# Performance work log

Measured on AMD Instinct MI355X. Metric: run time of the kernel, lower is better.

Reference implementation:

```python
import jax, jax.numpy as jnp
import numpy as np

H = 64      # hidden width of each MLP
M_STEPS = 64   # SDE steps (m)
N_SIM = 2048   # Monte-Carlo paths (n)
D = 128        # number of options (data_size)


def _mlp4(x, W1, b1, W2, b2, W3, b3):
    # x: [n, d, 4]; weights stacked over the 4 networks on axis 0 (k)
    h = jax.nn.relu(jnp.einsum('ndf,kfh->kndh', x, W1) + b1[:, None, None, :])
    h = jax.nn.relu(jnp.einsum('kndh,khg->kndg', h, W2) + b2[:, None, None, :])
    o = jnp.einsum('kndg,kgo->kndo', h, W3) + b3[:, None, None, :]
    return jnp.tanh(o)  # [4, n, d, 1]


def setup_inputs() -> dict:
    key = jax.random.key(0)
    ks = jax.random.split(key, 12)
    S0 = jax.random.uniform(ks[0], (D,), jnp.float32, 50.0, 150.0)
    K = jax.random.uniform(ks[1], (D,), jnp.float32, 50.0, 150.0)
    T = jax.random.uniform(ks[2], (D,), jnp.float32, 0.25, 2.0)
    rf = jnp.array([0.03], jnp.float32)
    V0 = jnp.array([0.04], jnp.float32)
    rho = jnp.array([-0.5], jnp.float32)
    Z1 = jax.random.normal(ks[3], (M_STEPS, N_SIM, D), jnp.float32)
    Z2raw = jax.random.normal(ks[4], (M_STEPS, N_SIM, D), jnp.float32)
    # 4 MLPs, layers [4, H, H, 1]
    W1 = jax.random.normal(ks[5], (4, 4, H), jnp.float32) / jnp.sqrt(4.0)
    b1 = jnp.zeros((4, H), jnp.float32)
    W2 = jax.random.normal(ks[6], (4, H, H), jnp.float32) / jnp.sqrt(float(H))
    b2 = jnp.zeros((4, H), jnp.float32)
    W3 = jax.random.normal(ks[7], (4, H, 1), jnp.float32) / jnp.sqrt(float(H))
    b3 = jnp.zeros((4, 1), jnp.float32)
    return {"S0": S0, "K": K, "T": T, "rf": rf, "V0": V0, "rho": rho,
            "Z1": Z1, "Z2raw": Z2raw,
            "W1": W1, "b1": b1, "W2": W2, "b2": b2, "W3": W3, "b3": b3}


def reference(S0, K, T, rf, V0, rho, Z1, Z2raw, W1, b1, W2, b2, W3, b3):
    m, n, d = Z1.shape
    dt = (T / m)[None, :, None]          # [1, d, 1]
    sdt = jnp.sqrt(dt)
    rho_s = rho[0]
    rf_s = rf[0]
    S = jnp.broadcast_to(S0[None, :, None], (n, d, 1))
    V = jnp.broadcast_to(V0[0], (n, d, 1))

    def step(carry, xs):
        S, V = carry
        j, z1, z2r = xs                    # z1, z2r: [n, d]
        z2 = rho_s * z1 + jnp.sqrt(1.0 - rho_s ** 2) * z2r
        feat = jnp.concatenate([
            S, V,
            jnp.broadcast_to(rf_s, S.shape),
            jnp.broadcast_to(dt * j, S.shape),
        ], axis=2)                          # [n, d, 4]
        N1, N2, N3, N4 = _mlp4(feat, W1, b1, W2, b2, W3, b3)
        Vn = V * (1.0 + N3 * dt + N4 * sdt * z2[..., None])
        Sn = S * (1.0 + N1 * dt + N2 * sdt * z1[..., None])
        return (Sn, Vn), None

    js = jnp.arange(m, dtype=jnp.float32)
    (S, V), _ = jax.lax.scan(step, (S, V), (js, Z1, Z2raw))
    S = S[..., 0]                            # [n, d]
    payoff = jnp.maximum(S - K[None, :], 0.0)
    P_pred = jnp.sum(jnp.exp(-rf_s * T)[None, :] * payoff, axis=0) / n
    return P_pred
```

## Files before the change

### kernel.cpp

```cpp
#include <hip/hip_runtime.h>
#include <math.h>

#define D_OPT   128
#define N_SIM   2048
#define M_STEPS 64
#define HID     64


typedef _Float16 f16x8 __attribute__((ext_vector_type(8)));
typedef _Float16 f16x2 __attribute__((ext_vector_type(2)));
typedef float    f32x4 __attribute__((ext_vector_type(4)));
typedef unsigned int u32;
typedef u32 u32x4 __attribute__((ext_vector_type(4)));

__device__ __forceinline__ u32 pk2u(float a, float b) {
#if __has_builtin(__builtin_amdgcn_cvt_pkrtz)
    return __builtin_bit_cast(u32, __builtin_amdgcn_cvt_pkrtz(a, b));
#else
    f16x2 p; p[0] = (_Float16)a; p[1] = (_Float16)b;
    return __builtin_bit_cast(u32, p);
#endif
}

__device__ __forceinline__ u32 pk_relu_cvt(float a, float b) {
    f16x2 p = __builtin_bit_cast(f16x2, pk2u(a, b));
    const f16x2 z = { (_Float16)0.0f, (_Float16)0.0f };
#if __has_builtin(__builtin_elementwise_max)
    p = __builtin_elementwise_max(p, z);
#else
    p[0] = p[0] > z[0] ? p[0] : z[0];
    p[1] = p[1] > z[1] ? p[1] : z[1];
#endif
    return __builtin_bit_cast(u32, p);
}

__global__ __launch_bounds__(256, 2) void nsde_kernel(
    const float* __restrict__ S0p, const float* __restrict__ Kp,
    const float* __restrict__ Tp,  const float* __restrict__ rfp,
    const float* __restrict__ V0p, const float* __restrict__ rhop,
    const float* __restrict__ Z1,  const float* __restrict__ Z2r,
    const float* __restrict__ W1,  const float* __restrict__ B1,
    const float* __restrict__ W2,  const float* __restrict__ B2,
    const float* __restrict__ W3,  const float* __restrict__ B3,
    float* __restrict__ out)
{
    __shared__ f32x4 nv_lds[2][64];
    __shared__ uint2 pkx[4][64];

    const int tid  = threadIdx.x;
    const int wave = tid >> 6;
    const int lane = tid & 63;
    const int q    = lane >> 4;
    const int mA   = lane & 15;
    const float rf = rfp[0];

    const float* w1g = W1 + wave * 256;
    const float* b1g = B1 + wave * 64;
    const float* w2g = W2 + wave * 4096;
    const float* b2g = B2 + wave * 64;
    const float* w3g = W3 + wave * 64;

    f16x8 A1[4];
    #pragma unroll
    for (int t = 0; t < 4; ++t) {
        f16x8 a;
        #pragma unroll
        for (int j = 0; j < 8; ++j) a[j] = (_Float16)0.0f;
        if (q == 0) {
            const int h = t * 16 + mA;
            a[0] = (_Float16)w1g[0 * 64 + h];
            a[1] = (_Float16)w1g[1 * 64 + h];
            a[2] = (_Float16)w1g[3 * 64 + h];
        }
        A1[t] = a;
    }

    f16x8 A2[4][2];
    #pragma unroll
    for (int gt = 0; gt < 4; ++gt)
        #pragma unroll
        for (int kt = 0; kt < 2; ++kt) {
            f16x8 a;
            #pragma unroll
            for (int j = 0; j < 8; ++j) {
                const int h1 = (2 * kt + (j >> 2)) * 16 + 4 * q + (j & 3);
                a[j] = (_Float16)w2g[h1 * 64 + gt * 16 + mA];
            }
            A2[gt][kt] = a;
        }

    f16x8 A3[2];
    #pragma unroll
    for (int kt = 0; kt < 2; ++kt) {
        f16x8 a;
        #pragma unroll
        for (int j = 0; j < 8; ++j) a[j] = (_Float16)0.0f;
        if (mA == 0) {
            #pragma unroll
            for (int j = 0; j < 8; ++j) {
                const int g = (2 * kt + (j >> 2)) * 16 + 4 * q + (j & 3);
                a[j] = (_Float16)w3g[g];
            }
        }
        A3[kt] = a;
    }

    f32x4 cinit1[4], cinit2[4], cinit3;
    #pragma unroll
    for (int t = 0; t < 4; ++t)
        #pragma unroll
        for (int r = 0; r < 4; ++r) {
            const int h = t * 16 + 4 * q + r;
            cinit1[t][r] = fmaf(rf, w1g[2 * 64 + h], b1g[h]);
            cinit2[t][r] = b2g[h];
        }
    const float b3 = B3[wave];
    cinit3[0] = b3; cinit3[1] = b3; cinit3[2] = b3; cinit3[3] = b3;

    const int ebase = blockIdx.x * 64;
    const int d_own = (ebase + lane) & (D_OPT - 1);
    const float dt_own  = Tp[d_own] * (1.0f / (float)M_STEPS);
    const float sdt_own = sqrtf(dt_own);

    float Sreg = S0p[d_own];
    float Vreg = V0p[0];
    {
        uint2 pk0;
        pk0.x = pk2u(Sreg, Vreg);
        pk0.y = pk2u(0.0f, 0.0f);
        pkx[wave][lane] = pk0;
    }

    const float rho   = rhop[0];
    const float rho_c = sqrtf(1.0f - rho * rho);
    const size_t estep = (size_t)N_SIM * D_OPT;
    const float* z1p = Z1  + (size_t)ebase + (size_t)lane;
    const float* z2p = Z2r + (size_t)ebase + (size_t)lane;

    #pragma unroll 1
    for (int s = 0; s < M_STEPS; ++s) {
        const float z1  = *z1p;
        const float z2r = *z2p;
        z1p += estep; z2p += estep;

        #pragma unroll
        for (int mt = 0; mt < 4; ++mt) {
            const uint2 pksv = pkx[wave][mt * 16 + mA];
            u32x4 b1u;
            b1u[0] = pksv.x;
            b1u[1] = pksv.y;
            b1u[2] = pksv.x;
            b1u[3] = pksv.x;
            const f16x8 B1f = __builtin_bit_cast(f16x8, b1u);

            u32x4 b2u[2];
            #pragma unroll
            for (int t = 0; t < 4; ++t) {
                const f32x4 acc = __builtin_amdgcn_mfma_f32_16x16x32_f16(
                                      A1[t], B1f, cinit1[t], 0, 0, 0);
                b2u[t >> 1][(t & 1) * 2 + 0] = pk_relu_cvt(acc[0], acc[1]);
                b2u[t >> 1][(t & 1) * 2 + 1] = pk_relu_cvt(acc[2], acc[3]);
            }
            const f16x8 B2f0 = __builtin_bit_cast(f16x8, b2u[0]);
            const f16x8 B2f1 = __builtin_bit_cast(f16x8, b2u[1]);

            u32x4 b3u[2];
            #pragma unroll
            for (int gt = 0; gt < 4; ++gt) {
                f32x4 acc = __builtin_amdgcn_mfma_f32_16x16x32_f16(
                                A2[gt][0], B2f0, cinit2[gt], 0, 0, 0);
                acc = __builtin_amdgcn_mfma_f32_16x16x32_f16(
                                A2[gt][1], B2f1, acc, 0, 0, 0);
                b3u[gt >> 1][(gt & 1) * 2 + 0] = pk_relu_cvt(acc[0], acc[1]);
                b3u[gt >> 1][(gt & 1) * 2 + 1] = pk_relu_cvt(acc[2], acc[3]);
            }

            f32x4 acc3 = __builtin_amdgcn_mfma_f32_16x16x32_f16(
                             A3[0], __builtin_bit_cast(f16x8, b3u[0]), cinit3, 0, 0, 0);
            acc3 = __builtin_amdgcn_mfma_f32_16x16x32_f16(
                             A3[1], __builtin_bit_cast(f16x8, b3u[1]), acc3, 0, 0, 0);

            if (q == 0)
                ((float*)&nv_lds[s & 1][mt * 16 + mA])[wave] = acc3[0];
        }

        __syncthreads();

        {
            const f32x4 o4 = nv_lds[s & 1][lane];
            const float e0 = __expf(2.0f * o4[0]);
            const float e1 = __expf(2.0f * o4[1]);
            const float e2 = __expf(2.0f * o4[2]);
            const float e3 = __expf(2.0f * o4[3]);
            const float N0 = 1.0f - 2.0f / (e0 + 1.0f);
            const float N1 = 1.0f - 2.0f / (e1 + 1.0f);
            const float N2 = 1.0f - 2.0f / (e2 + 1.0f);
            const float N3 = 1.0f - 2.0f / (e3 + 1.0f);
            const float z2 = fmaf(rho, z1, rho_c * z2r);
            const float fS = fmaf(N1 * sdt_own, z1, N0 * dt_own);
            const float fV = fmaf(N3 * sdt_own, z2, N2 * dt_own);
            Sreg = fmaf(Sreg, fS, Sreg);
            Vreg = fmaf(Vreg, fV, Vreg);
            uint2 pkn;
            pkn.x = pk2u(Sreg, Vreg);
            pkn.y = pk2u(dt_own * (float)(s + 1), 0.0f);
            pkx[wave][lane] = pkn;
        }
    }

    if (wave == 0) {
        const float Td  = dt_own * (float)M_STEPS;
        const float pay = fmaxf(Sreg - Kp[d_own], 0.0f);
        atomicAdd(&out[d_own], __expf(-rf * Td) * pay * (1.0f / (float)N_SIM));
    }
}

extern "C" void kernel_launch(void* const* d_in, const int* in_sizes, int n_in,
                              void* d_out, int out_size, void* d_ws, size_t ws_size,
                              hipStream_t stream)
{
    const float* S0  = (const float*)d_in[0];
    const float* K   = (const float*)d_in[1];
    const float* T   = (const float*)d_in[2];
    const float* rf  = (const float*)d_in[3];
    const float* V0  = (const float*)d_in[4];
    const float* rho = (const float*)d_in[5];
    const float* Z1  = (const float*)d_in[6];
    const float* Z2r = (const float*)d_in[7];
    const float* W1  = (const float*)d_in[8];
    const float* B1  = (const float*)d_in[9];
    const float* W2  = (const float*)d_in[10];
    const float* B2  = (const float*)d_in[11];
    const float* W3  = (const float*)d_in[12];
    const float* B3  = (const float*)d_in[13];
    float* out = (float*)d_out;

    hipMemsetAsync(out, 0, (size_t)out_size * sizeof(float), stream);

    const int total = N_SIM * D_OPT;
    const int grid  = total / 64;
    nsde_kernel<<<grid, 256, 0, stream>>>(S0, K, T, rf, V0, rho, Z1, Z2r,
                                          W1, B1, W2, B2, W3, B3, out);
}
```

Measured before the change: 831.9 us.

## Shrink layer-1 MFMA to 16x16x16 with bias folded into weights, raise occupancy

Layer 1 now uses the smaller 16x16x16 f16 MFMA. The constant rf*W1+b1 term is folded into a fourth weight column multiplied by a constant 1 input, so the per-tile cinit1 accumulators go away. The b3 bias moves into the post-sync epilogue, the output LDS layout becomes [wave][lane], the mt loop is only partly unrolled, and launch bounds ask for 4 blocks per CU. The aim is fewer registers for higher occupancy and less MFMA work in layer 1. The risk is extra spilling or a weaker schedule from the partial unroll, and the bias term is now held in f16.

```diff
diff --git a/kernel.cpp b/kernel.cpp
--- a/kernel.cpp
+++ b/kernel.cpp
@@ -8,9 +8,11 @@
 
 
 typedef _Float16 f16x8 __attribute__((ext_vector_type(8)));
+typedef _Float16 f16x4 __attribute__((ext_vector_type(4)));
 typedef _Float16 f16x2 __attribute__((ext_vector_type(2)));
 typedef float    f32x4 __attribute__((ext_vector_type(4)));
 typedef unsigned int u32;
+typedef u32 u32x2 __attribute__((ext_vector_type(2)));
 typedef u32 u32x4 __attribute__((ext_vector_type(4)));
 
 __device__ __forceinline__ u32 pk2u(float a, float b) {
@@ -34,7 +36,7 @@
     return __builtin_bit_cast(u32, p);
 }
 
-__global__ __launch_bounds__(256, 2) void nsde_kernel(
+__global__ __launch_bounds__(256, 4) void nsde_kernel(
     const float* __restrict__ S0p, const float* __restrict__ Kp,
     const float* __restrict__ Tp,  const float* __restrict__ rfp,
     const float* __restrict__ V0p, const float* __restrict__ rhop,
@@ -44,8 +46,8 @@
     const float* __restrict__ W3,  const float* __restrict__ B3,
     float* __restrict__ out)
 {
-    __shared__ f32x4 nv_lds[2][64];
-    __shared__ uint2 pkx[4][64];
+    __shared__ float nvp[2][4][64];
+    __shared__ u32x2 pkx[4][64];
 
     const int tid  = threadIdx.x;
     const int wave = tid >> 6;
@@ -60,17 +62,16 @@
     const float* b2g = B2 + wave * 64;
     const float* w3g = W3 + wave * 64;
 
-    f16x8 A1[4];
+    f16x4 A1[4];
     #pragma unroll
     for (int t = 0; t < 4; ++t) {
-        f16x8 a;
-        #pragma unroll
-        for (int j = 0; j < 8; ++j) a[j] = (_Float16)0.0f;
+        f16x4 a = { (_Float16)0.0f, (_Float16)0.0f, (_Float16)0.0f, (_Float16)0.0f };
         if (q == 0) {
             const int h = t * 16 + mA;
             a[0] = (_Float16)w1g[0 * 64 + h];
             a[1] = (_Float16)w1g[1 * 64 + h];
             a[2] = (_Float16)w1g[3 * 64 + h];
+            a[3] = (_Float16)fmaf(rf, w1g[2 * 64 + h], b1g[h]);
         }
         A1[t] = a;
     }
@@ -105,17 +106,15 @@
         A3[kt] = a;
     }
 
-    f32x4 cinit1[4], cinit2[4], cinit3;
+    f32x4 cinit2[4];
     #pragma unroll
     for (int t = 0; t < 4; ++t)
         #pragma unroll
-        for (int r = 0; r < 4; ++r) {
-            const int h = t * 16 + 4 * q + r;
-            cinit1[t][r] = fmaf(rf, w1g[2 * 64 + h], b1g[h]);
-            cinit2[t][r] = b2g[h];
-        }
-    const float b3 = B3[wave];
-    cinit3[0] = b3; cinit3[1] = b3; cinit3[2] = b3; cinit3[3] = b3;
+        for (int r = 0; r < 4; ++r)
+            cinit2[t][r] = b2g[t * 16 + 4 * q + r];
+    const f32x4 zc = { 0.0f, 0.0f, 0.0f, 0.0f };
+
+    const float b3n0 = B3[0], b3n1 = B3[1], b3n2 = B3[2], b3n3 = B3[3];
 
     const int ebase = blockIdx.x * 64;
     const int d_own = (ebase + lane) & (D_OPT - 1);
@@ -125,9 +124,9 @@
     float Sreg = S0p[d_own];
     float Vreg = V0p[0];
     {
-        uint2 pk0;
-        pk0.x = pk2u(Sreg, Vreg);
-        pk0.y = pk2u(0.0f, 0.0f);
+        u32x2 pk0;
+        pk0[0] = pk2u(Sreg, Vreg);
+        pk0[1] = pk2u(0.0f, 1.0f);
         pkx[wave][lane] = pk0;
     }
 
@@ -143,21 +142,16 @@
         const float z2r = *z2p;
         z1p += estep; z2p += estep;
 
-        #pragma unroll
+        #pragma unroll 2
         for (int mt = 0; mt < 4; ++mt) {
-            const uint2 pksv = pkx[wave][mt * 16 + mA];
-            u32x4 b1u;
-            b1u[0] = pksv.x;
-            b1u[1] = pksv.y;
-            b1u[2] = pksv.x;
-            b1u[3] = pksv.x;
-            const f16x8 B1f = __builtin_bit_cast(f16x8, b1u);
+            const u32x2 pksv = pkx[wave][mt * 16 + mA];
+            const f16x4 B1f = __builtin_bit_cast(f16x4, pksv);
 
             u32x4 b2u[2];
             #pragma unroll
             for (int t = 0; t < 4; ++t) {
-                const f32x4 acc = __builtin_amdgcn_mfma_f32_16x16x32_f16(
-                                      A1[t], B1f, cinit1[t], 0, 0, 0);
+                const f32x4 acc = __builtin_amdgcn_mfma_f32_16x16x16f16(
+                                      A1[t], B1f, zc, 0, 0, 0);
                 b2u[t >> 1][(t & 1) * 2 + 0] = pk_relu_cvt(acc[0], acc[1]);
                 b2u[t >> 1][(t & 1) * 2 + 1] = pk_relu_cvt(acc[2], acc[3]);
             }
@@ -176,22 +170,25 @@
             }
 
             f32x4 acc3 = __builtin_amdgcn_mfma_f32_16x16x32_f16(
-                             A3[0], __builtin_bit_cast(f16x8, b3u[0]), cinit3, 0, 0, 0);
+                             A3[0], __builtin_bit_cast(f16x8, b3u[0]), zc, 0, 0, 0);
             acc3 = __builtin_amdgcn_mfma_f32_16x16x32_f16(
                              A3[1], __builtin_bit_cast(f16x8, b3u[1]), acc3, 0, 0, 0);
 
             if (q == 0)
-                ((float*)&nv_lds[s & 1][mt * 16 + mA])[wave] = acc3[0];
+                nvp[s & 1][wave][mt * 16 + mA] = acc3[0];
         }
 
         __syncthreads();
 
         {
-            const f32x4 o4 = nv_lds[s & 1][lane];
-            const float e0 = __expf(2.0f * o4[0]);
-            const float e1 = __expf(2.0f * o4[1]);
-            const float e2 = __expf(2.0f * o4[2]);
-            const float e3 = __expf(2.0f * o4[3]);
+            const float o0 = nvp[s & 1][0][lane] + b3n0;
+            const float o1 = nvp[s & 1][1][lane] + b3n1;
+            const float o2 = nvp[s & 1][2][lane] + b3n2;
+            const float o3 = nvp[s & 1][3][lane] + b3n3;
+            const float e0 = __expf(2.0f * o0);
+            const float e1 = __expf(2.0f * o1);
+            const float e2 = __expf(2.0f * o2);
+            const float e3 = __expf(2.0f * o3);
             const float N0 = 1.0f - 2.0f / (e0 + 1.0f);
             const float N1 = 1.0f - 2.0f / (e1 + 1.0f);
             const float N2 = 1.0f - 2.0f / (e2 + 1.0f);
@@ -201,9 +198,9 @@
             const float fV = fmaf(N3 * sdt_own, z2, N2 * dt_own);
             Sreg = fmaf(Sreg, fS, Sreg);
             Vreg = fmaf(Vreg, fV, Vreg);
-            uint2 pkn;
-            pkn.x = pk2u(Sreg, Vreg);
-            pkn.y = pk2u(dt_own * (float)(s + 1), 0.0f);
+            u32x2 pkn;
+            pkn[0] = pk2u(Sreg, Vreg);
+            pkn[1] = pk2u(dt_own * (float)(s + 1), 1.0f);
             pkx[wave][lane] = pkn;
         }
     }
```

After: 817.8 us. Within noise of the previous version (-1.7%).
